# Kernel tuning notes

Hardware: AMD Instinct MI355X
Metric: run time of the kernel (lower is better)

## Reference

```python
import jax, jax.numpy as jnp
import numpy as np

OUT, IN = 4096, 4096
B, S = 2, 2048

def setup_inputs() -> dict:
    key = jax.random.key(0)
    k1, k2, k3, k4 = jax.random.split(key, 4)
    x = jax.random.normal(k1, (B, S, IN), dtype=jnp.float32)
    # symmetric int8 quantized weight [out, in]
    weight_q = jax.random.randint(k2, (OUT, IN), -128, 128, dtype=jnp.int32).astype(jnp.int8)
    # per-output-channel scale, small positive (like |w|_max/127)
    scale = (jax.random.uniform(k3, (1, OUT), dtype=jnp.float32) * 0.01 + 1e-4)
    bias = jax.random.normal(k4, (OUT,), dtype=jnp.float32)
    return {"x": x, "weight_q": weight_q, "scale": scale, "bias": bias}

def reference(x, weight_q, scale, bias):
    # out = (x_2d @ W_q^T (dequantized)) * scale + bias
    x2d = x.reshape(-1, x.shape[-1])                       # [B*S, in]
    w = weight_q.astype(x.dtype)                            # dequant cast [out, in]
    out = jnp.einsum('ni,oi->no', x2d, w) * scale           # [B*S, out] * [1, out]
    out = out.reshape(x.shape[:-1] + (out.shape[-1],))
    return out + bias
```

## Files before the change

kernel.cpp:

```cpp
#include <hip/hip_runtime.h>
#include <stdint.h>


#define M_DIM 4096
#define N_DIM 4096
#define K_DIM 4096
#define BM 256
#define BN 256
#define BK 32
#define KT_N (K_DIM / BK)
#define TILE_SHORTS 8192
#define BUF_SHORTS 16384
#define B_OFF 8192

typedef _Float16 f16x8 __attribute__((ext_vector_type(8)));
typedef __bf16   bf16x8v __attribute__((ext_vector_type(8)));
typedef float    f32x4 __attribute__((ext_vector_type(4)));

__device__ __forceinline__ unsigned short f32_f16_bits(float f) {
    _Float16 h = (_Float16)f;
    return __builtin_bit_cast(unsigned short, h);
}

__device__ __forceinline__ void gld16(const unsigned short* g, unsigned short* l) {
    __builtin_amdgcn_global_load_lds(
        (const __attribute__((address_space(1))) unsigned int*)g,
        (__attribute__((address_space(3))) unsigned int*)l,
        16, 0, 0);
}

__global__ __launch_bounds__(256) void cvt_x_f16(const float* __restrict__ x,
                                                 unsigned short* __restrict__ AT) {
    const int b  = blockIdx.x;
    const int mi = b >> 7;
    const int kt = b & 127;
    const int r  = threadIdx.x;

    const float* xp = x + (size_t)(mi * 256 + r) * K_DIM + kt * 32;
    unsigned short hh[32];
    #pragma unroll
    for (int j4 = 0; j4 < 8; ++j4) {
        float4 v = *(const float4*)(xp + j4 * 4);
        hh[j4*4+0] = f32_f16_bits(v.x);
        hh[j4*4+1] = f32_f16_bits(v.y);
        hh[j4*4+2] = f32_f16_bits(v.z);
        hh[j4*4+3] = f32_f16_bits(v.w);
    }
    unsigned short* o = AT + (size_t)(mi * KT_N + kt) * TILE_SHORTS + r * 8;
    #pragma unroll
    for (int ks = 0; ks < 4; ++ks) {
        uint4 p;
        p.x = (unsigned)hh[ks*8+0] | ((unsigned)hh[ks*8+1] << 16);
        p.y = (unsigned)hh[ks*8+2] | ((unsigned)hh[ks*8+3] << 16);
        p.z = (unsigned)hh[ks*8+4] | ((unsigned)hh[ks*8+5] << 16);
        p.w = (unsigned)hh[ks*8+6] | ((unsigned)hh[ks*8+7] << 16);
        *(uint4*)(o + ks * 2048) = p;
    }
}

__global__ __launch_bounds__(256) void cvt_w_f16(const int* __restrict__ wq,
                                                 unsigned short* __restrict__ BT) {
    const int b  = blockIdx.x;
    const int ni = b >> 7;
    const int kt = b & 127;
    const int c  = threadIdx.x;

    const int* wp = wq + (size_t)(ni * 256 + c) * K_DIM + kt * 32;
    unsigned short bb[32];
    #pragma unroll
    for (int j4 = 0; j4 < 8; ++j4) {
        int4 v = *(const int4*)(wp + j4 * 4);
        bb[j4*4+0] = f32_f16_bits((float)v.x);
        bb[j4*4+1] = f32_f16_bits((float)v.y);
        bb[j4*4+2] = f32_f16_bits((float)v.z);
        bb[j4*4+3] = f32_f16_bits((float)v.w);
    }
    unsigned short* ob = BT + (size_t)(ni * KT_N + kt) * TILE_SHORTS + c * 8;
    #pragma unroll
    for (int ks = 0; ks < 4; ++ks) {
        uint4 p;
        p.x = (unsigned)bb[ks*8+0] | ((unsigned)bb[ks*8+1] << 16);
        p.y = (unsigned)bb[ks*8+2] | ((unsigned)bb[ks*8+3] << 16);
        p.z = (unsigned)bb[ks*8+4] | ((unsigned)bb[ks*8+5] << 16);
        p.w = (unsigned)bb[ks*8+6] | ((unsigned)bb[ks*8+7] << 16);
        *(uint4*)(ob + ks * 2048) = p;
    }
}

__global__ __launch_bounds__(512, 2) void gemm_pipe(
    const unsigned short* __restrict__ AT,
    const unsigned short* __restrict__ BT,
    const float* __restrict__ scale, const float* __restrict__ bias,
    float* __restrict__ out)
{
    __shared__ unsigned short lds[3 * BUF_SHORTS];

    const int t    = threadIdx.x;
    const int lane = t & 63;
    const int wid  = t >> 6;
    const int wr   = wid >> 2;
    const int wc   = wid & 3;
    const int lr   = lane & 15;
    const int ksf  = lane >> 4;

    const int bid = blockIdx.x;
    const int swz = (bid & 7) * 32 + (bid >> 3);
    const int mi  = swz & 15;
    const int ni  = swz >> 4;

    const int lb0 = (t & ~63) * 8;
    const int lb1 = lb0 + 4096;
    const unsigned short* gA = AT + (size_t)mi * KT_N * TILE_SHORTS + t * 8;
    const unsigned short* gB = BT + (size_t)ni * KT_N * TILE_SHORTS + t * 8;

#define STAGE(bufbase, kt) do { \
    gld16(gA + (size_t)(kt) * TILE_SHORTS,        lds + (bufbase) + lb0); \
    gld16(gA + (size_t)(kt) * TILE_SHORTS + 4096, lds + (bufbase) + lb1); \
    gld16(gB + (size_t)(kt) * TILE_SHORTS,        lds + (bufbase) + B_OFF + lb0); \
    gld16(gB + (size_t)(kt) * TILE_SHORTS + 4096, lds + (bufbase) + B_OFF + lb1); \
} while (0)

    int offA[8], offB[4];
    #pragma unroll
    for (int m = 0; m < 8; ++m)
        offA[m] = (ksf * 256 + wr * 128 + m * 16 + lr) * 8;
    #pragma unroll
    for (int n = 0; n < 4; ++n)
        offB[n] = B_OFF + (ksf * 256 + wc * 64 + n * 16 + lr) * 8;

    f32x4 acc[8][4];
    #pragma unroll
    for (int m = 0; m < 8; ++m)
        #pragma unroll
        for (int n = 0; n < 4; ++n)
            acc[m][n] = (f32x4){0.f, 0.f, 0.f, 0.f};

    STAGE(0, 0);
    STAGE(BUF_SHORTS, 1);
    asm volatile("s_waitcnt vmcnt(4)" ::: "memory");
    __builtin_amdgcn_s_barrier();

    int curB = 0;
    int preB = 2 * BUF_SHORTS;

    for (int kt = 0; kt < KT_N; ++kt) {
        const unsigned short* Lb = lds + curB;

        f16x8 a4[8], b4[4];
        #pragma unroll
        for (int m = 0; m < 8; ++m) a4[m] = *(const f16x8*)(Lb + offA[m]);
        #pragma unroll
        for (int n = 0; n < 4; ++n) b4[n] = *(const f16x8*)(Lb + offB[n]);

        if (kt + 2 < KT_N) STAGE(preB, kt + 2);

        asm volatile("s_waitcnt lgkmcnt(0)" ::: "memory");
        __builtin_amdgcn_sched_barrier(0);
        __builtin_amdgcn_s_setprio(1);
        #pragma unroll
        for (int m = 0; m < 8; ++m)
            #pragma unroll
            for (int n = 0; n < 4; ++n)
                acc[m][n] = __builtin_amdgcn_mfma_f32_16x16x32_f16(a4[m], b4[n], acc[m][n], 0, 0, 0);
        __builtin_amdgcn_s_setprio(0);

        if (kt + 2 < KT_N) asm volatile("s_waitcnt vmcnt(4)" ::: "memory");
        else               asm volatile("s_waitcnt vmcnt(0)" ::: "memory");
        __builtin_amdgcn_s_barrier();

        curB = (curB == 2 * BUF_SHORTS) ? 0 : curB + BUF_SHORTS;
        preB = (preB == 2 * BUF_SHORTS) ? 0 : preB + BUF_SHORTS;
    }
#undef STAGE

    #pragma unroll
    for (int n = 0; n < 4; ++n) {
        const int col = ni * BN + wc * 64 + n * 16 + lr;
        const float sc = scale[col];
        const float bi = bias[col];
        #pragma unroll
        for (int m = 0; m < 8; ++m) {
            const int r0 = mi * BM + wr * 128 + m * 16 + ksf * 4;
            #pragma unroll
            for (int j = 0; j < 4; ++j)
                out[(size_t)(r0 + j) * N_DIM + col] = acc[m][n][j] * sc + bi;
        }
    }
}

__device__ __forceinline__ unsigned short f32_bf16_rne(float f) {
    unsigned u = __float_as_uint(f);
    u += 0x7FFFu + ((u >> 16) & 1u);
    return (unsigned short)(u >> 16);
}

__device__ __forceinline__ void cvt2(float a, float b, unsigned& hi2, unsigned& lo2) {
    unsigned short ha = f32_bf16_rne(a), hb = f32_bf16_rne(b);
    float fa = __uint_as_float((unsigned)ha << 16);
    float fb = __uint_as_float((unsigned)hb << 16);
    unsigned short la = f32_bf16_rne(a - fa), lb = f32_bf16_rne(b - fb);
    hi2 = (unsigned)ha | ((unsigned)hb << 16);
    lo2 = (unsigned)la | ((unsigned)lb << 16);
}

__global__ __launch_bounds__(256) void gemm_fb(
    const float* __restrict__ X, const int* __restrict__ Wq,
    const float* __restrict__ scale, const float* __restrict__ bias,
    float* __restrict__ out)
{
    __shared__ unsigned short sAh[4 * 128 * 8];
    __shared__ unsigned short sAl[4 * 128 * 8];
    __shared__ unsigned short sB [4 * 128 * 8];

    const int t    = threadIdx.x;
    const int lane = t & 63;
    const int wid  = t >> 6;
    const int brow = blockIdx.y * 128;
    const int bcol = blockIdx.x * 128;

    const int c1 = t,        c2 = t + 256;
    const int r1 = c1 & 127, s1 = c1 >> 7;
    const int r2 = c2 & 127, s2 = c2 >> 7;

    const int wr  = wid >> 1, wc = wid & 1;
    const int lr  = lane & 15;
    const int ksf = lane >> 4;

    f32x4 acc[4][4];
    #pragma unroll
    for (int m = 0; m < 4; ++m)
        #pragma unroll
        for (int n = 0; n < 4; ++n)
            acc[m][n] = (f32x4){0.f, 0.f, 0.f, 0.f};

    for (int k0 = 0; k0 < K_DIM; k0 += 32) {
        #pragma unroll
        for (int cc = 0; cc < 2; ++cc) {
            const int c = cc ? c2 : c1;
            const int r = cc ? r2 : r1;
            const int s = cc ? s2 : s1;
            const float* xa = X + (size_t)(brow + r) * K_DIM + k0 + s * 8;
            float4 v0 = *(const float4*)(xa);
            float4 v1 = *(const float4*)(xa + 4);
            uint4 hv, lv;
            cvt2(v0.x, v0.y, hv.x, lv.x);
            cvt2(v0.z, v0.w, hv.y, lv.y);
            cvt2(v1.x, v1.y, hv.z, lv.z);
            cvt2(v1.z, v1.w, hv.w, lv.w);
            *(uint4*)(sAh + c * 8) = hv;
            *(uint4*)(sAl + c * 8) = lv;

            const int* wa = Wq + (size_t)(bcol + r) * K_DIM + k0 + s * 8;
            int4 w0 = *(const int4*)(wa);
            int4 w1 = *(const int4*)(wa + 4);
            uint4 wv;
            wv.x = (unsigned)f32_bf16_rne((float)w0.x) | ((unsigned)f32_bf16_rne((float)w0.y) << 16);
            wv.y = (unsigned)f32_bf16_rne((float)w0.z) | ((unsigned)f32_bf16_rne((float)w0.w) << 16);
            wv.z = (unsigned)f32_bf16_rne((float)w1.x) | ((unsigned)f32_bf16_rne((float)w1.y) << 16);
            wv.w = (unsigned)f32_bf16_rne((float)w1.z) | ((unsigned)f32_bf16_rne((float)w1.w) << 16);
            *(uint4*)(sB + c * 8) = wv;
        }
        __syncthreads();

        bf16x8v ah[4], al[4], bb[4];
        #pragma unroll
        for (int m = 0; m < 4; ++m) {
            const int row = wr * 64 + m * 16 + lr;
            ah[m] = *(const bf16x8v*)(sAh + (ksf * 128 + row) * 8);
            al[m] = *(const bf16x8v*)(sAl + (ksf * 128 + row) * 8);
        }
        #pragma unroll
        for (int n = 0; n < 4; ++n) {
            const int row = wc * 64 + n * 16 + lr;
            bb[n] = *(const bf16x8v*)(sB + (ksf * 128 + row) * 8);
        }

        #pragma unroll
        for (int m = 0; m < 4; ++m)
            #pragma unroll
            for (int n = 0; n < 4; ++n) {
                acc[m][n] = __builtin_amdgcn_mfma_f32_16x16x32_bf16(ah[m], bb[n], acc[m][n], 0, 0, 0);
                acc[m][n] = __builtin_amdgcn_mfma_f32_16x16x32_bf16(al[m], bb[n], acc[m][n], 0, 0, 0);
            }
        __syncthreads();
    }

    #pragma unroll
    for (int n = 0; n < 4; ++n) {
        const int col = bcol + wc * 64 + n * 16 + lr;
        const float sc = scale[col];
        const float bi = bias[col];
        #pragma unroll
        for (int m = 0; m < 4; ++m) {
            const int r0 = brow + wr * 64 + m * 16 + ksf * 4;
            #pragma unroll
            for (int j = 0; j < 4; ++j)
                out[(size_t)(r0 + j) * N_DIM + col] = acc[m][n][j] * sc + bi;
        }
    }
}

extern "C" void kernel_launch(void* const* d_in, const int* in_sizes, int n_in,
                              void* d_out, int out_size, void* d_ws, size_t ws_size,
                              hipStream_t stream) {
    const float* x     = (const float*)d_in[0];
    const int*   wq    = (const int*)d_in[1];
    const float* scale = (const float*)d_in[2];
    const float* bias  = (const float*)d_in[3];
    float*       out   = (float*)d_out;

    const size_t planeElems = (size_t)M_DIM * K_DIM;
    const size_t planeBytes = planeElems * sizeof(unsigned short);

    if (ws_size >= 2 * planeBytes) {
        unsigned short* AT = (unsigned short*)d_ws;
        unsigned short* BT = AT + planeElems;
        cvt_x_f16<<<2048, 256, 0, stream>>>(x, AT);
        cvt_w_f16<<<2048, 256, 0, stream>>>(wq, BT);
        gemm_pipe<<<(M_DIM / BM) * (N_DIM / BN), 512, 0, stream>>>(AT, BT, scale, bias, out);
    } else {
        dim3 grid(N_DIM / 128, M_DIM / 128);
        gemm_fb<<<grid, 256, 0, stream>>>(x, wq, scale, bias, out);
    }
}
```

Measured before the change: 160.1 us.

## Deepen LDS pipeline to four buffers and split k-step into two phases

Grows the LDS ring from three to four stages so tiles are prefetched three k-steps ahead. Each k-step is split into two halves: A and B global loads are issued separately, and the A-fragment LDS reads for each half are interleaved with the MFMA work of that half. The aim is to hide more global-memory latency and spread LDS traffic across the compute. The cost is more LDS per block (128KB for two blocks per CU is near the limit) and extra barriers per iteration, which may reduce occupancy or add synchronisation stalls.

```diff
diff --git a/kernel.cpp b/kernel.cpp
--- a/kernel.cpp
+++ b/kernel.cpp
@@ -93,7 +93,7 @@
     const float* __restrict__ scale, const float* __restrict__ bias,
     float* __restrict__ out)
 {
-    __shared__ unsigned short lds[3 * BUF_SHORTS];
+    __shared__ unsigned short lds[4 * BUF_SHORTS];
 
     const int t    = threadIdx.x;
     const int lane = t & 63;
@@ -113,9 +113,11 @@
     const unsigned short* gA = AT + (size_t)mi * KT_N * TILE_SHORTS + t * 8;
     const unsigned short* gB = BT + (size_t)ni * KT_N * TILE_SHORTS + t * 8;
 
-#define STAGE(bufbase, kt) do { \
+#define STAGE_A(bufbase, kt) do { \
     gld16(gA + (size_t)(kt) * TILE_SHORTS,        lds + (bufbase) + lb0); \
     gld16(gA + (size_t)(kt) * TILE_SHORTS + 4096, lds + (bufbase) + lb1); \
+} while (0)
+#define STAGE_B(bufbase, kt) do { \
     gld16(gB + (size_t)(kt) * TILE_SHORTS,        lds + (bufbase) + B_OFF + lb0); \
     gld16(gB + (size_t)(kt) * TILE_SHORTS + 4096, lds + (bufbase) + B_OFF + lb1); \
 } while (0)
@@ -135,43 +137,57 @@
         for (int n = 0; n < 4; ++n)
             acc[m][n] = (f32x4){0.f, 0.f, 0.f, 0.f};
 
-    STAGE(0, 0);
-    STAGE(BUF_SHORTS, 1);
-    asm volatile("s_waitcnt vmcnt(4)" ::: "memory");
+    STAGE_A(0, 0);              STAGE_B(0, 0);
+    STAGE_A(BUF_SHORTS, 1);     STAGE_B(BUF_SHORTS, 1);
+    STAGE_A(2 * BUF_SHORTS, 2); STAGE_B(2 * BUF_SHORTS, 2);
+    asm volatile("s_waitcnt vmcnt(8)" ::: "memory");
     __builtin_amdgcn_s_barrier();
 
-    int curB = 0;
-    int preB = 2 * BUF_SHORTS;
-
     for (int kt = 0; kt < KT_N; ++kt) {
-        const unsigned short* Lb = lds + curB;
+        const unsigned short* Lb = lds + (kt & 3) * BUF_SHORTS;
+        const int nst   = kt + 3;
+        const bool dost = nst < KT_N;
+        const int stB   = (nst & 3) * BUF_SHORTS;
 
         f16x8 a4[8], b4[4];
         #pragma unroll
-        for (int m = 0; m < 8; ++m) a4[m] = *(const f16x8*)(Lb + offA[m]);
-        #pragma unroll
         for (int n = 0; n < 4; ++n) b4[n] = *(const f16x8*)(Lb + offB[n]);
-
-        if (kt + 2 < KT_N) STAGE(preB, kt + 2);
-
+        #pragma unroll
+        for (int m = 0; m < 4; ++m) a4[m] = *(const f16x8*)(Lb + offA[m]);
+        if (dost) STAGE_A(stB, nst);
+        __builtin_amdgcn_s_barrier();
         asm volatile("s_waitcnt lgkmcnt(0)" ::: "memory");
         __builtin_amdgcn_sched_barrier(0);
         __builtin_amdgcn_s_setprio(1);
         #pragma unroll
-        for (int m = 0; m < 8; ++m)
+        for (int m = 0; m < 4; ++m)
             #pragma unroll
             for (int n = 0; n < 4; ++n)
                 acc[m][n] = __builtin_amdgcn_mfma_f32_16x16x32_f16(a4[m], b4[n], acc[m][n], 0, 0, 0);
         __builtin_amdgcn_s_setprio(0);
-
-        if (kt + 2 < KT_N) asm volatile("s_waitcnt vmcnt(4)" ::: "memory");
-        else               asm volatile("s_waitcnt vmcnt(0)" ::: "memory");
         __builtin_amdgcn_s_barrier();
 
-        curB = (curB == 2 * BUF_SHORTS) ? 0 : curB + BUF_SHORTS;
-        preB = (preB == 2 * BUF_SHORTS) ? 0 : preB + BUF_SHORTS;
-    }
-#undef STAGE
+        #pragma unroll
+        for (int m = 4; m < 8; ++m) a4[m] = *(const f16x8*)(Lb + offA[m]);
+        if (dost) STAGE_B(stB, nst);
+        __builtin_amdgcn_s_barrier();
+        asm volatile("s_waitcnt lgkmcnt(0)" ::: "memory");
+        __builtin_amdgcn_sched_barrier(0);
+        __builtin_amdgcn_s_setprio(1);
+        #pragma unroll
+        for (int m = 4; m < 8; ++m)
+            #pragma unroll
+            for (int n = 0; n < 4; ++n)
+                acc[m][n] = __builtin_amdgcn_mfma_f32_16x16x32_f16(a4[m], b4[n], acc[m][n], 0, 0, 0);
+        __builtin_amdgcn_s_setprio(0);
+
+        if (kt + 3 < KT_N)      asm volatile("s_waitcnt vmcnt(8)" ::: "memory");
+        else if (kt + 2 < KT_N) asm volatile("s_waitcnt vmcnt(4)" ::: "memory");
+        else if (kt + 1 < KT_N) asm volatile("s_waitcnt vmcnt(0)" ::: "memory");
+        __builtin_amdgcn_s_barrier();
+    }
+#undef STAGE_A
+#undef STAGE_B
 
     #pragma unroll
     for (int n = 0; n < 4; ++n) {
```

After: 164.3 us. 1.03x slower.

## Shrink GEMM block tile to 256x128 with 256 threads, two blocks per CU

Applied to the files above, without the earlier changes.

Changes the main GEMM block tile from 256x256 with 8 waves to 256x128 with 4 waves. The grid doubles to 512 blocks, so each CU can hold two independent blocks whose barriers are not synchronised with each other. The pre-converted weight layout and the cvt_w kernel are reworked to match 128-column tiles. The global-to-LDS staging now issues 6 loads per stage, and the vmcnt waits are updated to match. The B fragments are now read from LDS before the A fragments. The cost is less operand reuse per block and more total traffic from global memory or L2.

```diff
diff --git a/kernel.cpp b/kernel.cpp
--- a/kernel.cpp
+++ b/kernel.cpp
@@ -6,11 +6,12 @@
 #define N_DIM 4096
 #define K_DIM 4096
 #define BM 256
-#define BN 256
+#define BN 128
 #define BK 32
 #define KT_N (K_DIM / BK)
-#define TILE_SHORTS 8192
-#define BUF_SHORTS 16384
+#define A_TILE_SHORTS 8192
+#define B_TILE_SHORTS 4096
+#define BUF_SHORTS 12288
 #define B_OFF 8192
 
 typedef _Float16 f16x8 __attribute__((ext_vector_type(8)));
@@ -46,7 +47,7 @@
         hh[j4*4+2] = f32_f16_bits(v.z);
         hh[j4*4+3] = f32_f16_bits(v.w);
     }
-    unsigned short* o = AT + (size_t)(mi * KT_N + kt) * TILE_SHORTS + r * 8;
+    unsigned short* o = AT + (size_t)(mi * KT_N + kt) * A_TILE_SHORTS + r * 8;
     #pragma unroll
     for (int ks = 0; ks < 4; ++ks) {
         uint4 p;
@@ -60,12 +61,14 @@
 
 __global__ __launch_bounds__(256) void cvt_w_f16(const int* __restrict__ wq,
                                                  unsigned short* __restrict__ BT) {
-    const int b  = blockIdx.x;
-    const int ni = b >> 7;
-    const int kt = b & 127;
-    const int c  = threadIdx.x;
-
-    const int* wp = wq + (size_t)(ni * 256 + c) * K_DIM + kt * 32;
+    const int b   = blockIdx.x;
+    const int ni  = b >> 6;
+    const int kt2 = b & 63;
+    const int t   = threadIdx.x;
+    const int c   = t & 127;
+    const int kt  = kt2 * 2 + (t >> 7);
+
+    const int* wp = wq + (size_t)(ni * 128 + c) * K_DIM + kt * 32;
     unsigned short bb[32];
     #pragma unroll
     for (int j4 = 0; j4 < 8; ++j4) {
@@ -75,7 +78,7 @@
         bb[j4*4+2] = f32_f16_bits((float)v.z);
         bb[j4*4+3] = f32_f16_bits((float)v.w);
     }
-    unsigned short* ob = BT + (size_t)(ni * KT_N + kt) * TILE_SHORTS + c * 8;
+    unsigned short* ob = BT + (size_t)(ni * KT_N + kt) * B_TILE_SHORTS + c * 8;
     #pragma unroll
     for (int ks = 0; ks < 4; ++ks) {
         uint4 p;
@@ -83,11 +86,11 @@
         p.y = (unsigned)bb[ks*8+2] | ((unsigned)bb[ks*8+3] << 16);
         p.z = (unsigned)bb[ks*8+4] | ((unsigned)bb[ks*8+5] << 16);
         p.w = (unsigned)bb[ks*8+6] | ((unsigned)bb[ks*8+7] << 16);
-        *(uint4*)(ob + ks * 2048) = p;
-    }
-}
-
-__global__ __launch_bounds__(512, 2) void gemm_pipe(
+        *(uint4*)(ob + ks * 1024) = p;
+    }
+}
+
+__global__ __launch_bounds__(256, 2) void gemm_pipe(
     const unsigned short* __restrict__ AT,
     const unsigned short* __restrict__ BT,
     const float* __restrict__ scale, const float* __restrict__ bias,
@@ -98,26 +101,29 @@
     const int t    = threadIdx.x;
     const int lane = t & 63;
     const int wid  = t >> 6;
-    const int wr   = wid >> 2;
-    const int wc   = wid & 3;
+    const int wr   = wid >> 1;
+    const int wc   = wid & 1;
     const int lr   = lane & 15;
     const int ksf  = lane >> 4;
 
     const int bid = blockIdx.x;
-    const int swz = (bid & 7) * 32 + (bid >> 3);
+    const int swz = (bid & 7) * 64 + (bid >> 3);
     const int mi  = swz & 15;
     const int ni  = swz >> 4;
 
-    const int lb0 = (t & ~63) * 8;
-    const int lb1 = lb0 + 4096;
-    const unsigned short* gA = AT + (size_t)mi * KT_N * TILE_SHORTS + t * 8;
-    const unsigned short* gB = BT + (size_t)ni * KT_N * TILE_SHORTS + t * 8;
-
-#define STAGE(bufbase, kt) do { \
-    gld16(gA + (size_t)(kt) * TILE_SHORTS,        lds + (bufbase) + lb0); \
-    gld16(gA + (size_t)(kt) * TILE_SHORTS + 4096, lds + (bufbase) + lb1); \
-    gld16(gB + (size_t)(kt) * TILE_SHORTS,        lds + (bufbase) + B_OFF + lb0); \
-    gld16(gB + (size_t)(kt) * TILE_SHORTS + 4096, lds + (bufbase) + B_OFF + lb1); \
+    const int lbA = (t & ~63) * 8;
+    const unsigned short* gA = AT + (size_t)mi * KT_N * A_TILE_SHORTS + t * 8;
+    const unsigned short* gB = BT + (size_t)ni * KT_N * B_TILE_SHORTS + t * 8;
+
+#define STAGE(bufbase, kt) do {                                               \
+    _Pragma("unroll")                                                         \
+    for (int j = 0; j < 4; ++j)                                               \
+        gld16(gA + (size_t)(kt) * A_TILE_SHORTS + j * 2048,                   \
+              lds + (bufbase) + lbA + j * 2048);                              \
+    _Pragma("unroll")                                                         \
+    for (int j = 0; j < 2; ++j)                                               \
+        gld16(gB + (size_t)(kt) * B_TILE_SHORTS + j * 2048,                   \
+              lds + (bufbase) + B_OFF + lbA + j * 2048);                      \
 } while (0)
 
     int offA[8], offB[4];
@@ -126,7 +132,7 @@
         offA[m] = (ksf * 256 + wr * 128 + m * 16 + lr) * 8;
     #pragma unroll
     for (int n = 0; n < 4; ++n)
-        offB[n] = B_OFF + (ksf * 256 + wc * 64 + n * 16 + lr) * 8;
+        offB[n] = B_OFF + (ksf * 128 + wc * 64 + n * 16 + lr) * 8;
 
     f32x4 acc[8][4];
     #pragma unroll
@@ -137,7 +143,7 @@
 
     STAGE(0, 0);
     STAGE(BUF_SHORTS, 1);
-    asm volatile("s_waitcnt vmcnt(4)" ::: "memory");
+    asm volatile("s_waitcnt vmcnt(6)" ::: "memory");
     __builtin_amdgcn_s_barrier();
 
     int curB = 0;
@@ -148,9 +154,9 @@
 
         f16x8 a4[8], b4[4];
         #pragma unroll
+        for (int n = 0; n < 4; ++n) b4[n] = *(const f16x8*)(Lb + offB[n]);
+        #pragma unroll
         for (int m = 0; m < 8; ++m) a4[m] = *(const f16x8*)(Lb + offA[m]);
-        #pragma unroll
-        for (int n = 0; n < 4; ++n) b4[n] = *(const f16x8*)(Lb + offB[n]);
 
         if (kt + 2 < KT_N) STAGE(preB, kt + 2);
 
@@ -164,7 +170,7 @@
                 acc[m][n] = __builtin_amdgcn_mfma_f32_16x16x32_f16(a4[m], b4[n], acc[m][n], 0, 0, 0);
         __builtin_amdgcn_s_setprio(0);
 
-        if (kt + 2 < KT_N) asm volatile("s_waitcnt vmcnt(4)" ::: "memory");
+        if (kt + 2 < KT_N) asm volatile("s_waitcnt vmcnt(6)" ::: "memory");
         else               asm volatile("s_waitcnt vmcnt(0)" ::: "memory");
         __builtin_amdgcn_s_barrier();
 
@@ -317,7 +323,7 @@
         unsigned short* BT = AT + planeElems;
         cvt_x_f16<<<2048, 256, 0, stream>>>(x, AT);
         cvt_w_f16<<<2048, 256, 0, stream>>>(wq, BT);
-        gemm_pipe<<<(M_DIM / BM) * (N_DIM / BN), 512, 0, stream>>>(AT, BT, scale, bias, out);
+        gemm_pipe<<<(M_DIM / BM) * (N_DIM / BN), 256, 0, stream>>>(AT, BT, scale, bias, out);
     } else {
         dim3 grid(N_DIM / 128, M_DIM / 128);
         gemm_fb<<<grid, 256, 0, stream>>>(x, wq, scale, bias, out);
```

Measured after the change: 154.4 us (median of 3 runs). 3.6% less time.

## Use BK=64 double-buffered tiles with four-phase interleaved load/MFMA schedule

Applied to the files above, without the earlier changes.

Doubles the K tile to 64, switches from triple to double buffering of a larger LDS tile, and splits each iteration into four quadrant phases that interleave LDS fragment reads, half-tile global prefetches and MFMA bursts with barriers between them. The conversion kernels are reworked to emit the new half-split tile layout. The aim is to hide global-to-LDS latency and LDS read latency behind MFMA work, similar to ping-pong style schedules. In exchange there are more barriers per iteration, and occupancy drops to one block per CU because of the larger LDS footprint.

```diff
diff --git a/kernel.cpp b/kernel.cpp
--- a/kernel.cpp
+++ b/kernel.cpp
@@ -5,13 +5,11 @@
 #define M_DIM 4096
 #define N_DIM 4096
 #define K_DIM 4096
-#define BM 256
-#define BN 256
-#define BK 32
-#define KT_N (K_DIM / BK)
-#define TILE_SHORTS 8192
-#define BUF_SHORTS 16384
-#define B_OFF 8192
+#define KT_N 64
+#define TILE_SH 16384
+#define HALF_SH 8192
+#define BUF_SH 32768
+#define BSEC 16384
 
 typedef _Float16 f16x8 __attribute__((ext_vector_type(8)));
 typedef __bf16   bf16x8v __attribute__((ext_vector_type(8)));
@@ -32,68 +30,70 @@
 __global__ __launch_bounds__(256) void cvt_x_f16(const float* __restrict__ x,
                                                  unsigned short* __restrict__ AT) {
     const int b  = blockIdx.x;
-    const int mi = b >> 7;
-    const int kt = b & 127;
+    const int mi = b >> 6;
+    const int kt = b & 63;
     const int r  = threadIdx.x;
 
-    const float* xp = x + (size_t)(mi * 256 + r) * K_DIM + kt * 32;
-    unsigned short hh[32];
-    #pragma unroll
-    for (int j4 = 0; j4 < 8; ++j4) {
+    const float* xp = x + (size_t)(mi * 256 + r) * K_DIM + kt * 64;
+    unsigned short hh[64];
+    #pragma unroll
+    for (int j4 = 0; j4 < 16; ++j4) {
         float4 v = *(const float4*)(xp + j4 * 4);
         hh[j4*4+0] = f32_f16_bits(v.x);
         hh[j4*4+1] = f32_f16_bits(v.y);
         hh[j4*4+2] = f32_f16_bits(v.z);
         hh[j4*4+3] = f32_f16_bits(v.w);
     }
-    unsigned short* o = AT + (size_t)(mi * KT_N + kt) * TILE_SHORTS + r * 8;
-    #pragma unroll
-    for (int ks = 0; ks < 4; ++ks) {
+    unsigned short* o = AT + (size_t)(mi * KT_N + kt) * TILE_SH
+                      + (r >> 7) * HALF_SH + (r & 127) * 8;
+    #pragma unroll
+    for (int ks = 0; ks < 8; ++ks) {
         uint4 p;
         p.x = (unsigned)hh[ks*8+0] | ((unsigned)hh[ks*8+1] << 16);
         p.y = (unsigned)hh[ks*8+2] | ((unsigned)hh[ks*8+3] << 16);
         p.z = (unsigned)hh[ks*8+4] | ((unsigned)hh[ks*8+5] << 16);
         p.w = (unsigned)hh[ks*8+6] | ((unsigned)hh[ks*8+7] << 16);
-        *(uint4*)(o + ks * 2048) = p;
+        *(uint4*)(o + ks * 1024) = p;
     }
 }
 
 __global__ __launch_bounds__(256) void cvt_w_f16(const int* __restrict__ wq,
                                                  unsigned short* __restrict__ BT) {
     const int b  = blockIdx.x;
-    const int ni = b >> 7;
-    const int kt = b & 127;
+    const int ni = b >> 6;
+    const int kt = b & 63;
     const int c  = threadIdx.x;
 
-    const int* wp = wq + (size_t)(ni * 256 + c) * K_DIM + kt * 32;
-    unsigned short bb[32];
-    #pragma unroll
-    for (int j4 = 0; j4 < 8; ++j4) {
+    const int* wp = wq + (size_t)(ni * 256 + c) * K_DIM + kt * 64;
+    unsigned short bb[64];
+    #pragma unroll
+    for (int j4 = 0; j4 < 16; ++j4) {
         int4 v = *(const int4*)(wp + j4 * 4);
         bb[j4*4+0] = f32_f16_bits((float)v.x);
         bb[j4*4+1] = f32_f16_bits((float)v.y);
         bb[j4*4+2] = f32_f16_bits((float)v.z);
         bb[j4*4+3] = f32_f16_bits((float)v.w);
     }
-    unsigned short* ob = BT + (size_t)(ni * KT_N + kt) * TILE_SHORTS + c * 8;
-    #pragma unroll
-    for (int ks = 0; ks < 4; ++ks) {
+    unsigned short* ob = BT + (size_t)(ni * KT_N + kt) * TILE_SH
+                       + (c >> 7) * HALF_SH + (c & 127) * 8;
+    #pragma unroll
+    for (int ks = 0; ks < 8; ++ks) {
         uint4 p;
         p.x = (unsigned)bb[ks*8+0] | ((unsigned)bb[ks*8+1] << 16);
         p.y = (unsigned)bb[ks*8+2] | ((unsigned)bb[ks*8+3] << 16);
         p.z = (unsigned)bb[ks*8+4] | ((unsigned)bb[ks*8+5] << 16);
         p.w = (unsigned)bb[ks*8+6] | ((unsigned)bb[ks*8+7] << 16);
-        *(uint4*)(ob + ks * 2048) = p;
-    }
-}
-
-__global__ __launch_bounds__(512, 2) void gemm_pipe(
+        *(uint4*)(ob + ks * 1024) = p;
+    }
+}
+
+__global__ __launch_bounds__(512, 1) void gemm_pipe(
     const unsigned short* __restrict__ AT,
     const unsigned short* __restrict__ BT,
     const float* __restrict__ scale, const float* __restrict__ bias,
     float* __restrict__ out)
 {
-    __shared__ unsigned short lds[3 * BUF_SHORTS];
+    __shared__ unsigned short lds[2 * BUF_SH];
 
     const int t    = threadIdx.x;
     const int lane = t & 63;
@@ -108,25 +108,20 @@
     const int mi  = swz & 15;
     const int ni  = swz >> 4;
 
-    const int lb0 = (t & ~63) * 8;
-    const int lb1 = lb0 + 4096;
-    const unsigned short* gA = AT + (size_t)mi * KT_N * TILE_SHORTS + t * 8;
-    const unsigned short* gB = BT + (size_t)ni * KT_N * TILE_SHORTS + t * 8;
-
-#define STAGE(bufbase, kt) do { \
-    gld16(gA + (size_t)(kt) * TILE_SHORTS,        lds + (bufbase) + lb0); \
-    gld16(gA + (size_t)(kt) * TILE_SHORTS + 4096, lds + (bufbase) + lb1); \
-    gld16(gB + (size_t)(kt) * TILE_SHORTS,        lds + (bufbase) + B_OFF + lb0); \
-    gld16(gB + (size_t)(kt) * TILE_SHORTS + 4096, lds + (bufbase) + B_OFF + lb1); \
+    const int lbA = (t & ~63) * 8;
+    const unsigned short* gA = AT + (size_t)mi * KT_N * TILE_SH + t * 8;
+    const unsigned short* gB = BT + (size_t)ni * KT_N * TILE_SH + t * 8;
+
+#define STG(bufb, sec, h, src, tile) do {                                     \
+    gld16((src) + (size_t)(tile) * TILE_SH + (h) * HALF_SH,                   \
+          lds + (bufb) + (sec) + (h) * HALF_SH + lbA);                        \
+    gld16((src) + (size_t)(tile) * TILE_SH + (h) * HALF_SH + 4096,            \
+          lds + (bufb) + (sec) + (h) * HALF_SH + lbA + 4096);                 \
 } while (0)
 
-    int offA[8], offB[4];
-    #pragma unroll
-    for (int m = 0; m < 8; ++m)
-        offA[m] = (ksf * 256 + wr * 128 + m * 16 + lr) * 8;
-    #pragma unroll
-    for (int n = 0; n < 4; ++n)
-        offB[n] = B_OFF + (ksf * 256 + wc * 64 + n * 16 + lr) * 8;
+    const int baseA = wr * HALF_SH + ksf * 1024 + lr * 8;
+    const int baseB = BSEC + (wc >> 1) * HALF_SH + ksf * 1024
+                    + ((wc & 1) * 64 + lr) * 8;
 
     f32x4 acc[8][4];
     #pragma unroll
@@ -135,52 +130,116 @@
         for (int n = 0; n < 4; ++n)
             acc[m][n] = (f32x4){0.f, 0.f, 0.f, 0.f};
 
-    STAGE(0, 0);
-    STAGE(BUF_SHORTS, 1);
+    f16x8 a0[8], a1[8], bq[8];
+
+    STG(0,      BSEC, 0, gB, 0);
+    STG(0,      0,    0, gA, 0);
+    STG(0,      BSEC, 1, gB, 0);
+    STG(0,      0,    1, gA, 0);
+    STG(BUF_SH, BSEC, 0, gB, 1);
+    STG(BUF_SH, 0,    0, gA, 1);
     asm volatile("s_waitcnt vmcnt(4)" ::: "memory");
     __builtin_amdgcn_s_barrier();
 
-    int curB = 0;
-    int preB = 2 * BUF_SHORTS;
-
     for (int kt = 0; kt < KT_N; ++kt) {
+        const int curB = (kt & 1) * BUF_SH;
+        const int othB = BUF_SH - curB;
         const unsigned short* Lb = lds + curB;
 
-        f16x8 a4[8], b4[4];
-        #pragma unroll
-        for (int m = 0; m < 8; ++m) a4[m] = *(const f16x8*)(Lb + offA[m]);
-        #pragma unroll
-        for (int n = 0; n < 4; ++n) b4[n] = *(const f16x8*)(Lb + offB[n]);
-
-        if (kt + 2 < KT_N) STAGE(preB, kt + 2);
-
+        #pragma unroll
+        for (int n = 0; n < 2; ++n)
+            #pragma unroll
+            for (int kk = 0; kk < 2; ++kk)
+                bq[n*2+kk] = *(const f16x8*)(Lb + baseB + n*128 + kk*4096);
+        #pragma unroll
+        for (int m = 0; m < 4; ++m)
+            #pragma unroll
+            for (int kk = 0; kk < 2; ++kk)
+                a0[m*2+kk] = *(const f16x8*)(Lb + baseA + m*128 + kk*4096);
+        if (kt + 1 < KT_N) STG(othB, BSEC, 1, gB, kt + 1);
+        __builtin_amdgcn_s_barrier();
         asm volatile("s_waitcnt lgkmcnt(0)" ::: "memory");
         __builtin_amdgcn_sched_barrier(0);
         __builtin_amdgcn_s_setprio(1);
         #pragma unroll
-        for (int m = 0; m < 8; ++m)
-            #pragma unroll
-            for (int n = 0; n < 4; ++n)
-                acc[m][n] = __builtin_amdgcn_mfma_f32_16x16x32_f16(a4[m], b4[n], acc[m][n], 0, 0, 0);
+        for (int m = 0; m < 4; ++m)
+            #pragma unroll
+            for (int n = 0; n < 2; ++n)
+                #pragma unroll
+                for (int kk = 0; kk < 2; ++kk)
+                    acc[m][n] = __builtin_amdgcn_mfma_f32_16x16x32_f16(
+                        a0[m*2+kk], bq[n*2+kk], acc[m][n], 0, 0, 0);
         __builtin_amdgcn_s_setprio(0);
-
+        __builtin_amdgcn_s_barrier();
+
+        #pragma unroll
+        for (int n = 2; n < 4; ++n)
+            #pragma unroll
+            for (int kk = 0; kk < 2; ++kk)
+                bq[n*2+kk] = *(const f16x8*)(Lb + baseB + n*128 + kk*4096);
+        if (kt + 1 < KT_N) STG(othB, 0, 1, gA, kt + 1);
+        __builtin_amdgcn_s_barrier();
+        asm volatile("s_waitcnt lgkmcnt(0)" ::: "memory");
+        __builtin_amdgcn_sched_barrier(0);
+        __builtin_amdgcn_s_setprio(1);
+        #pragma unroll
+        for (int m = 0; m < 4; ++m)
+            #pragma unroll
+            for (int n = 2; n < 4; ++n)
+                #pragma unroll
+                for (int kk = 0; kk < 2; ++kk)
+                    acc[m][n] = __builtin_amdgcn_mfma_f32_16x16x32_f16(
+                        a0[m*2+kk], bq[n*2+kk], acc[m][n], 0, 0, 0);
+        __builtin_amdgcn_s_setprio(0);
+        __builtin_amdgcn_s_barrier();
+
+        #pragma unroll
+        for (int m = 0; m < 4; ++m)
+            #pragma unroll
+            for (int kk = 0; kk < 2; ++kk)
+                a1[m*2+kk] = *(const f16x8*)(Lb + baseA + (m+4)*128 + kk*4096);
+        if (kt + 2 < KT_N) STG(curB, BSEC, 0, gB, kt + 2);
+        __builtin_amdgcn_s_barrier();
+        asm volatile("s_waitcnt lgkmcnt(0)" ::: "memory");
+        __builtin_amdgcn_sched_barrier(0);
+        __builtin_amdgcn_s_setprio(1);
+        #pragma unroll
+        for (int m = 4; m < 8; ++m)
+            #pragma unroll
+            for (int n = 0; n < 2; ++n)
+                #pragma unroll
+                for (int kk = 0; kk < 2; ++kk)
+                    acc[m][n] = __builtin_amdgcn_mfma_f32_16x16x32_f16(
+                        a1[(m-4)*2+kk], bq[n*2+kk], acc[m][n], 0, 0, 0);
+        __builtin_amdgcn_s_setprio(0);
+        __builtin_amdgcn_s_barrier();
+
+        if (kt + 2 < KT_N) STG(curB, 0, 0, gA, kt + 2);
+        __builtin_amdgcn_s_barrier();
+        __builtin_amdgcn_s_setprio(1);
+        #pragma unroll
+        for (int m = 4; m < 8; ++m)
+            #pragma unroll
+            for (int n = 2; n < 4; ++n)
+                #pragma unroll
+                for (int kk = 0; kk < 2; ++kk)
+                    acc[m][n] = __builtin_amdgcn_mfma_f32_16x16x32_f16(
+                        a1[(m-4)*2+kk], bq[n*2+kk], acc[m][n], 0, 0, 0);
+        __builtin_amdgcn_s_setprio(0);
         if (kt + 2 < KT_N) asm volatile("s_waitcnt vmcnt(4)" ::: "memory");
         else               asm volatile("s_waitcnt vmcnt(0)" ::: "memory");
         __builtin_amdgcn_s_barrier();
-
-        curB = (curB == 2 * BUF_SHORTS) ? 0 : curB + BUF_SHORTS;
-        preB = (preB == 2 * BUF_SHORTS) ? 0 : preB + BUF_SHORTS;
-    }
-#undef STAGE
+    }
+#undef STG
 
     #pragma unroll
     for (int n = 0; n < 4; ++n) {
-        const int col = ni * BN + wc * 64 + n * 16 + lr;
+        const int col = ni * 256 + wc * 64 + n * 16 + lr;
         const float sc = scale[col];
         const float bi = bias[col];
         #pragma unroll
         for (int m = 0; m < 8; ++m) {
-            const int r0 = mi * BM + wr * 128 + m * 16 + ksf * 4;
+            const int r0 = mi * 256 + wr * 128 + m * 16 + ksf * 4;
             #pragma unroll
             for (int j = 0; j < 4; ++j)
                 out[(size_t)(r0 + j) * N_DIM + col] = acc[m][n][j] * sc + bi;
@@ -315,9 +374,9 @@
     if (ws_size >= 2 * planeBytes) {
         unsigned short* AT = (unsigned short*)d_ws;
         unsigned short* BT = AT + planeElems;
-        cvt_x_f16<<<2048, 256, 0, stream>>>(x, AT);
-        cvt_w_f16<<<2048, 256, 0, stream>>>(wq, BT);
-        gemm_pipe<<<(M_DIM / BM) * (N_DIM / BN), 512, 0, stream>>>(AT, BT, scale, bias, out);
+        cvt_x_f16<<<1024, 256, 0, stream>>>(x, AT);
+        cvt_w_f16<<<1024, 256, 0, stream>>>(wq, BT);
+        gemm_pipe<<<256, 512, 0, stream>>>(AT, BT, scale, bias, out);
     } else {
         dim3 grid(N_DIM / 128, M_DIM / 128);
         gemm_fb<<<grid, 256, 0, stream>>>(x, wq, scale, bias, out);
```

Measured after the change: 156.8 us. -2.1%, faster.
